# Performance work log

Hardware: AMD Instinct MI355X
Metric: run time of the kernel (lower is better)

Reference implementation:

```python
import jax, jax.numpy as jnp
import numpy as np

B, T, H, A = 64, 512, 1024, 300


def setup_inputs() -> dict:
    key = jax.random.key(0)
    ks = jax.random.split(key, 12)
    s = 0.02  # weight init scale
    return {
        "hidden": jax.random.normal(ks[0], (B, T, H), jnp.float32),
        "aspect": jax.random.normal(ks[1], (B, 1, A), jnp.float32),
        # torch Linear stores weight as [out_features, in_features]
        "W_h": jax.random.normal(ks[2], (H, H), jnp.float32) * s,
        "b_h": jax.random.normal(ks[3], (H,), jnp.float32) * s,
        "W_v": jax.random.normal(ks[4], (A, A), jnp.float32) * s,
        "b_v": jax.random.normal(ks[5], (A,), jnp.float32) * s,
        "w_w": jax.random.normal(ks[6], (1, H + A), jnp.float32) * s,
        "w_b": jax.random.normal(ks[7], (1,), jnp.float32) * s,
        "W_p": jax.random.normal(ks[8], (H, H), jnp.float32) * s,
        "b_p": jax.random.normal(ks[9], (H,), jnp.float32) * s,
        "W_x": jax.random.normal(ks[10], (H, H), jnp.float32) * s,
        "b_x": jax.random.normal(ks[11], (H,), jnp.float32) * s,
    }


def reference(hidden, aspect, W_h, b_h, W_v, b_v, w_w, w_b, W_p, b_p, W_x, b_x):
    # transformed aspect: [B, 1, A], repeated along seq dim -> [B, T, A]
    tv = aspect @ W_v.T + b_v
    rep_v = jnp.broadcast_to(tv, (hidden.shape[0], hidden.shape[1], tv.shape[-1]))
    # M = tanh(concat(W_h(hidden), repeated_v)) : [B, T, H+A]
    M = jnp.tanh(jnp.concatenate([hidden @ W_h.T + b_h, rep_v], axis=-1))
    # additive attention scores -> softmax over T
    scores = jnp.einsum("bts,os->bto", M, w_w)[..., 0] + w_b[0]  # [B, T]
    alpha = jax.nn.softmax(scores, axis=-1)
    # weighted sum r = alpha^T @ hidden : [B, 1, H]
    r = jnp.einsum("bt,bth->bh", alpha, hidden)[:, None, :]
    # NOTE: faithful to original torch broadcasting quirk:
    # [B,1,H] + [B,H] broadcasts to [B,B,H]
    output = jnp.tanh((r @ W_p.T + b_p) + (hidden[:, -1, :] @ W_x.T + b_x))
    return output
```

## Files before the change

### kernel.cpp

```cpp
#include <hip/hip_runtime.h>
#include <hip/hip_bf16.h>
#include <stdint.h>

#define B_DIM 64
#define T_DIM 512
#define H_DIM 1024
#define K_DIM 1024
#define M_DIM (B_DIM * T_DIM)

typedef __bf16 bf16x8 __attribute__((ext_vector_type(8)));
typedef float f32x4 __attribute__((ext_vector_type(4)));

__device__ __forceinline__ float tanh_fast(float x) {
  float e = __expf(2.0f * x);
  return 1.0f - 2.0f / (e + 1.0f);
}

__device__ __forceinline__ float bf2f(unsigned short u) {
  return __uint_as_float(((unsigned int)u) << 16);
}

__device__ __forceinline__ void async_cp16(const void* gp, void* lp) {
  __builtin_amdgcn_global_load_lds(
      reinterpret_cast<const __attribute__((address_space(1))) uint32_t*>(
          reinterpret_cast<uintptr_t>(gp)),
      reinterpret_cast<__attribute__((address_space(3))) uint32_t*>(
          reinterpret_cast<uintptr_t>(lp)),
      16, 0, 0);
}

__global__ void prep_kernel(const float* __restrict__ hidden, __bf16* __restrict__ hidBf,
                            const float* __restrict__ Wh, __bf16* __restrict__ whBf,
                            float* __restrict__ scores) {
  const int bid = blockIdx.x, tid = threadIdx.x;
  if (bid < 32768) {
    int i = bid * 256 + tid;
    float4 v = reinterpret_cast<const float4*>(hidden)[i];
    union { __bf16 b[4]; uint2 u; } o;
    o.b[0] = (__bf16)v.x; o.b[1] = (__bf16)v.y; o.b[2] = (__bf16)v.z; o.b[3] = (__bf16)v.w;
    reinterpret_cast<uint2*>(hidBf)[i] = o.u;
  } else if (bid < 33792) {
    int i = (bid - 32768) * 256 + tid;
    float4 v = reinterpret_cast<const float4*>(Wh)[i];
    union { __bf16 b[4]; uint2 u; } o;
    o.b[0] = (__bf16)v.x; o.b[1] = (__bf16)v.y; o.b[2] = (__bf16)v.z; o.b[3] = (__bf16)v.w;
    reinterpret_cast<uint2*>(whBf)[i] = o.u;
  } else {
    int i = (bid - 33792) * 256 + tid;
    reinterpret_cast<float4*>(scores)[i] = make_float4(0.f, 0.f, 0.f, 0.f);
  }
}

#define GM_BK 64
__global__ __launch_bounds__(256, 2) void gemm_scores_kernel(
    const __bf16* __restrict__ A, const __bf16* __restrict__ Bm,
    const float* __restrict__ bh, const float* __restrict__ ww,
    float* __restrict__ scores) {
  __shared__ __attribute__((aligned(16))) __bf16 lA[256 * GM_BK];
  __shared__ __attribute__((aligned(16))) __bf16 lB[128 * GM_BK];

  const int tid = threadIdx.x;
  const int bid = blockIdx.x;
  const int m0 = (bid & 127) * 256;
  const int n0 = (bid >> 7) * 128;

  const int wv = tid >> 6;
  const int lane = tid & 63;
  const int wm = wv & 1, wn = wv >> 1;
  const int r16 = lane & 15, quad = lane >> 4;

  f32x4 acc[8][4] = {};

  const __bf16* gA[8]; __bf16* lAd[8];
#pragma unroll
  for (int j = 0; j < 8; ++j) {
    int c = j * 256 + tid;
    int row = c >> 3;
    int p = c & 7;
    int kc = p ^ ((row >> 1) & 7);
    gA[j] = A + (size_t)(m0 + row) * K_DIM + kc * 8;
    lAd[j] = &lA[c * 8];
  }
  const __bf16* gB[4]; __bf16* lBd[4];
#pragma unroll
  for (int j = 0; j < 4; ++j) {
    int c = j * 256 + tid;
    int row = c >> 3;
    int p = c & 7;
    int kc = p ^ ((row >> 1) & 7);
    gB[j] = Bm + (size_t)(n0 + row) * K_DIM + kc * 8;
    lBd[j] = &lB[c * 8];
  }

  const int sw = r16 >> 1;
  const __bf16* pa[2]; const __bf16* pb[2];
#pragma unroll
  for (int kk = 0; kk < 2; ++kk) {
    pa[kk] = &lA[(wm * 128 + r16) * GM_BK + ((kk * 4 + quad) ^ sw) * 8];
    pb[kk] = &lB[(wn * 64 + r16) * GM_BK + ((kk * 4 + quad) ^ sw) * 8];
  }

#pragma unroll
  for (int k0 = 0; k0 < K_DIM; k0 += GM_BK) {
#pragma unroll
    for (int j = 0; j < 8; ++j) async_cp16(gA[j] + k0, lAd[j]);
#pragma unroll
    for (int j = 0; j < 4; ++j) async_cp16(gB[j] + k0, lBd[j]);
    __syncthreads();
#pragma unroll
    for (int kk = 0; kk < 2; ++kk) {
      bf16x8 bfr[4];
#pragma unroll
      for (int ni = 0; ni < 4; ++ni)
        bfr[ni] = *reinterpret_cast<const bf16x8*>(pb[kk] + ni * 16 * GM_BK);
      bf16x8 af[8];
#pragma unroll
      for (int mi = 0; mi < 8; ++mi)
        af[mi] = *reinterpret_cast<const bf16x8*>(pa[kk] + mi * 16 * GM_BK);
#pragma unroll
      for (int mi = 0; mi < 8; ++mi)
#pragma unroll
        for (int ni = 0; ni < 4; ++ni)
          acc[mi][ni] = __builtin_amdgcn_mfma_f32_16x16x32_bf16(af[mi], bfr[ni], acc[mi][ni], 0, 0, 0);
    }
    __syncthreads();
  }

  float bhv[4], wwv[4];
#pragma unroll
  for (int ni = 0; ni < 4; ++ni) {
    int n = n0 + wn * 64 + ni * 16 + r16;
    bhv[ni] = bh[n];
    wwv[ni] = ww[n];
  }
#pragma unroll
  for (int mi = 0; mi < 8; ++mi) {
#pragma unroll
    for (int rg = 0; rg < 4; ++rg) {
      float s = 0.f;
#pragma unroll
      for (int ni = 0; ni < 4; ++ni)
        s += tanh_fast(acc[mi][ni][rg] + bhv[ni]) * wwv[ni];
      s += __shfl_xor(s, 1, 16);
      s += __shfl_xor(s, 2, 16);
      s += __shfl_xor(s, 4, 16);
      s += __shfl_xor(s, 8, 16);
      if (r16 == 0) {
        int m = m0 + wm * 128 + mi * 16 + quad * 4 + rg;
        atomicAdd(&scores[m], s);
      }
    }
  }
}

__global__ void wsum_kernel(const float* __restrict__ scores,
                            const __bf16* __restrict__ hiddenBf,
                            float* __restrict__ r8) {
  __shared__ float al[64];
  __shared__ float red[8];
  const int bid = blockIdx.x, tid = threadIdx.x;
  const int b = bid >> 3, tc = bid & 7;
  const int wv = tid >> 6, lane = tid & 63;
  float v0 = scores[b * T_DIM + tid];
  float v1 = scores[b * T_DIM + 256 + tid];
  float mx = fmaxf(v0, v1);
#pragma unroll
  for (int off = 1; off < 64; off <<= 1) mx = fmaxf(mx, __shfl_xor(mx, off, 64));
  if (lane == 0) red[wv] = mx;
  __syncthreads();
  mx = fmaxf(fmaxf(red[0], red[1]), fmaxf(red[2], red[3]));
  float e0 = __expf(v0 - mx), e1 = __expf(v1 - mx);
  float s = e0 + e1;
#pragma unroll
  for (int off = 1; off < 64; off <<= 1) s += __shfl_xor(s, off, 64);
  if (lane == 0) red[4 + wv] = s;
  __syncthreads();
  float inv = 1.0f / (red[4] + red[5] + red[6] + red[7]);
  if (tid < 64) al[tid] = __expf(scores[b * T_DIM + tc * 64 + tid] - mx) * inv;
  __syncthreads();
  const __bf16* hp = hiddenBf + (size_t)b * T_DIM * H_DIM + (size_t)tc * 64 * H_DIM + tid * 4;
  float4 acc = make_float4(0.f, 0.f, 0.f, 0.f);
#pragma unroll 8
  for (int t = 0; t < 64; ++t) {
    float a = al[t];
    ushort4 u = *reinterpret_cast<const ushort4*>(hp + (size_t)t * H_DIM);
    acc.x += a * bf2f(u.x);
    acc.y += a * bf2f(u.y);
    acc.z += a * bf2f(u.z);
    acc.w += a * bf2f(u.w);
  }
  *reinterpret_cast<float4*>(r8 + (size_t)(b * 8 + tc) * H_DIM + tid * 4) = acc;
}

#define IG 4
__global__ void rowvec2_kernel(const float* __restrict__ r8,
                               const float* __restrict__ hidden,
                               const float* __restrict__ W_p, const float* __restrict__ b_p,
                               const float* __restrict__ W_x, const float* __restrict__ b_x,
                               float* __restrict__ rp, float* __restrict__ xq) {
  __shared__ __attribute__((aligned(16))) float sv[IG][H_DIM];
  const int h0 = blockIdx.x * 64;
  const int i0 = blockIdx.y * IG;
  const int which = blockIdx.z;
  const int tid = threadIdx.x;
  const float* W = which ? W_x : W_p;
  const float* bias = which ? b_x : b_p;
  float* dst = which ? xq : rp;
  if (which == 0) {
#pragma unroll
    for (int ii = 0; ii < IG; ++ii) {
      const float* src = r8 + (size_t)(i0 + ii) * 8 * H_DIM + tid * 4;
      float4 a = *reinterpret_cast<const float4*>(src);
#pragma unroll
      for (int tc = 1; tc < 8; ++tc) {
        float4 v = *reinterpret_cast<const float4*>(src + (size_t)tc * H_DIM);
        a.x += v.x; a.y += v.y; a.z += v.z; a.w += v.w;
      }
      *reinterpret_cast<float4*>(&sv[ii][tid * 4]) = a;
    }
  } else {
#pragma unroll
    for (int ii = 0; ii < IG; ++ii) {
      const float* src = hidden + (size_t)(i0 + ii) * T_DIM * H_DIM +
                         (size_t)(T_DIM - 1) * H_DIM + tid * 4;
      *reinterpret_cast<float4*>(&sv[ii][tid * 4]) = *reinterpret_cast<const float4*>(src);
    }
  }
  __syncthreads();
  const int hl = tid >> 2;
  const int kq = tid & 3;
  const float* wr = W + (size_t)(h0 + hl) * H_DIM + kq * 4;
  float acc[IG] = {};
#pragma unroll 8
  for (int j = 0; j < 64; ++j) {
    float4 w4 = *reinterpret_cast<const float4*>(wr + j * 16);
#pragma unroll
    for (int ii = 0; ii < IG; ++ii) {
      float4 s4 = *reinterpret_cast<const float4*>(&sv[ii][kq * 4 + j * 16]);
      acc[ii] += w4.x * s4.x + w4.y * s4.y + w4.z * s4.z + w4.w * s4.w;
    }
  }
#pragma unroll
  for (int ii = 0; ii < IG; ++ii) {
    acc[ii] += __shfl_xor(acc[ii], 1, 4);
    acc[ii] += __shfl_xor(acc[ii], 2, 4);
  }
  if (kq == 0) {
    float bb = bias[h0 + hl];
#pragma unroll
    for (int ii = 0; ii < IG; ++ii)
      dst[(size_t)(i0 + ii) * H_DIM + h0 + hl] = acc[ii] + bb;
  }
}

__global__ void final_kernel(const float* __restrict__ rp, const float* __restrict__ xq,
                             float* __restrict__ out) {
  int idx = blockIdx.x * 256 + threadIdx.x;
  int e = idx * 4;
  int i = e >> 16;
  int j = (e >> 10) & 63;
  int h = e & 1023;
  float4 a = *reinterpret_cast<const float4*>(&rp[i * H_DIM + h]);
  float4 b = *reinterpret_cast<const float4*>(&xq[j * H_DIM + h]);
  float4 o;
  o.x = tanh_fast(a.x + b.x);
  o.y = tanh_fast(a.y + b.y);
  o.z = tanh_fast(a.z + b.z);
  o.w = tanh_fast(a.w + b.w);
  *reinterpret_cast<float4*>(&out[e]) = o;
}

extern "C" void kernel_launch(void* const* d_in, const int* in_sizes, int n_in,
                              void* d_out, int out_size, void* d_ws, size_t ws_size,
                              hipStream_t stream) {
  const float* hidden = (const float*)d_in[0];
  const float* W_h = (const float*)d_in[2];
  const float* b_h = (const float*)d_in[3];
  const float* w_w = (const float*)d_in[6];
  const float* W_p = (const float*)d_in[8];
  const float* b_p = (const float*)d_in[9];
  const float* W_x = (const float*)d_in[10];
  const float* b_x = (const float*)d_in[11];
  float* out = (float*)d_out;

  char* ws = (char*)d_ws;
  __bf16* hidBf = (__bf16*)ws;
  __bf16* whBf = (__bf16*)(ws + 67108864);
  float* r8 = (float*)(ws + 67108864);
  float* scores = (float*)(ws + 69206016);
  float* rpB = (float*)(ws + 69337088);
  float* xqB = (float*)(ws + 69599232);

  prep_kernel<<<33824, 256, 0, stream>>>(hidden, hidBf, W_h, whBf, scores);

  gemm_scores_kernel<<<1024, 256, 0, stream>>>(hidBf, whBf, b_h, w_w, scores);

  wsum_kernel<<<512, 256, 0, stream>>>(scores, hidBf, r8);

  rowvec2_kernel<<<dim3(H_DIM / 64, B_DIM / IG, 2), 256, 0, stream>>>(
      r8, hidden, W_p, b_p, W_x, b_x, rpB, xqB);

  final_kernel<<<(B_DIM * B_DIM * H_DIM / 4) / 256, 256, 0, stream>>>(rpB, xqB, out);
}
```

Before: 344.3 us.

## Fuse all stages into one persistent kernel with grid-wide barriers

Replaces the five separate launches (convert, GEMM+scores, softmax-weighted sum, row-vector GEMVs, final tanh) with a single persistent kernel of 512 blocks. The stages are separated by atomic-counter grid barriers, and shared memory is reused through a union. Each block now loops over two GEMM tiles and over grid-strided chunks for the elementwise phases. The aim is to remove kernel launch gaps and tail effects between stages. In exchange it relies on all blocks being co-resident, adds a memset launch for the counters, and the barrier spin has a timeout that could silently break ordering.

```diff
diff --git a/kernel.cpp b/kernel.cpp
--- a/kernel.cpp
+++ b/kernel.cpp
@@ -7,6 +7,10 @@
 #define H_DIM 1024
 #define K_DIM 1024
 #define M_DIM (B_DIM * T_DIM)
+#define GM_BK 64
+#define IG 4
+#define NBLK 512
+#define NTHR (NBLK * 256)
 
 typedef __bf16 bf16x8 __attribute__((ext_vector_type(8)));
 typedef float f32x4 __attribute__((ext_vector_type(4)));
@@ -29,245 +33,277 @@
       16, 0, 0);
 }
 
-__global__ void prep_kernel(const float* __restrict__ hidden, __bf16* __restrict__ hidBf,
-                            const float* __restrict__ Wh, __bf16* __restrict__ whBf,
-                            float* __restrict__ scores) {
-  const int bid = blockIdx.x, tid = threadIdx.x;
-  if (bid < 32768) {
-    int i = bid * 256 + tid;
-    float4 v = reinterpret_cast<const float4*>(hidden)[i];
-    union { __bf16 b[4]; uint2 u; } o;
-    o.b[0] = (__bf16)v.x; o.b[1] = (__bf16)v.y; o.b[2] = (__bf16)v.z; o.b[3] = (__bf16)v.w;
-    reinterpret_cast<uint2*>(hidBf)[i] = o.u;
-  } else if (bid < 33792) {
-    int i = (bid - 32768) * 256 + tid;
-    float4 v = reinterpret_cast<const float4*>(Wh)[i];
-    union { __bf16 b[4]; uint2 u; } o;
-    o.b[0] = (__bf16)v.x; o.b[1] = (__bf16)v.y; o.b[2] = (__bf16)v.z; o.b[3] = (__bf16)v.w;
-    reinterpret_cast<uint2*>(whBf)[i] = o.u;
-  } else {
-    int i = (bid - 33792) * 256 + tid;
-    reinterpret_cast<float4*>(scores)[i] = make_float4(0.f, 0.f, 0.f, 0.f);
-  }
-}
-
-#define GM_BK 64
-__global__ __launch_bounds__(256, 2) void gemm_scores_kernel(
-    const __bf16* __restrict__ A, const __bf16* __restrict__ Bm,
-    const float* __restrict__ bh, const float* __restrict__ ww,
-    float* __restrict__ scores) {
-  __shared__ __attribute__((aligned(16))) __bf16 lA[256 * GM_BK];
-  __shared__ __attribute__((aligned(16))) __bf16 lB[128 * GM_BK];
-
+__device__ __forceinline__ void cvt4(const float4& v, uint2* dst) {
+  union { __bf16 b[4]; uint2 u; } o;
+  o.b[0] = (__bf16)v.x; o.b[1] = (__bf16)v.y; o.b[2] = (__bf16)v.z; o.b[3] = (__bf16)v.w;
+  *dst = o.u;
+}
+
+__device__ __forceinline__ void grid_barrier(unsigned* cnt, int k) {
+  __syncthreads();
+  if (threadIdx.x == 0) {
+    __threadfence();
+    __hip_atomic_fetch_add(&cnt[k], 1u, __ATOMIC_RELEASE, __HIP_MEMORY_SCOPE_AGENT);
+    unsigned spins = 0;
+    while (__hip_atomic_load(&cnt[k], __ATOMIC_ACQUIRE, __HIP_MEMORY_SCOPE_AGENT) <
+           (unsigned)NBLK) {
+      __builtin_amdgcn_s_sleep(8);
+      if (++spins > (1u << 20)) break;
+    }
+    __threadfence();
+  }
+  __syncthreads();
+}
+
+union SharedU {
+  struct { __bf16 lA[256 * GM_BK]; __bf16 lB[128 * GM_BK]; } g;
+  struct { float al[64]; float red[8]; } w;
+  float sv[IG][H_DIM];
+};
+
+__global__ __launch_bounds__(256, 2) void mega_kernel(
+    const float* __restrict__ hidden, __bf16* __restrict__ hidBf,
+    const float* __restrict__ W_h, __bf16* __restrict__ whBf,
+    float* __restrict__ scores, const float* __restrict__ b_h,
+    const float* __restrict__ w_w, float* __restrict__ r8,
+    const float* __restrict__ W_p, const float* __restrict__ b_p,
+    const float* __restrict__ W_x, const float* __restrict__ b_x,
+    float* __restrict__ rp, float* __restrict__ xq, float* __restrict__ out,
+    unsigned* __restrict__ barcnt) {
+  __shared__ __attribute__((aligned(16))) SharedU sh;
   const int tid = threadIdx.x;
   const int bid = blockIdx.x;
-  const int m0 = (bid & 127) * 256;
-  const int n0 = (bid >> 7) * 128;
-
-  const int wv = tid >> 6;
-  const int lane = tid & 63;
-  const int wm = wv & 1, wn = wv >> 1;
-  const int r16 = lane & 15, quad = lane >> 4;
-
-  f32x4 acc[8][4] = {};
-
-  const __bf16* gA[8]; __bf16* lAd[8];
-#pragma unroll
-  for (int j = 0; j < 8; ++j) {
-    int c = j * 256 + tid;
-    int row = c >> 3;
-    int p = c & 7;
-    int kc = p ^ ((row >> 1) & 7);
-    gA[j] = A + (size_t)(m0 + row) * K_DIM + kc * 8;
-    lAd[j] = &lA[c * 8];
-  }
-  const __bf16* gB[4]; __bf16* lBd[4];
-#pragma unroll
-  for (int j = 0; j < 4; ++j) {
-    int c = j * 256 + tid;
-    int row = c >> 3;
-    int p = c & 7;
-    int kc = p ^ ((row >> 1) & 7);
-    gB[j] = Bm + (size_t)(n0 + row) * K_DIM + kc * 8;
-    lBd[j] = &lB[c * 8];
-  }
-
-  const int sw = r16 >> 1;
-  const __bf16* pa[2]; const __bf16* pb[2];
-#pragma unroll
-  for (int kk = 0; kk < 2; ++kk) {
-    pa[kk] = &lA[(wm * 128 + r16) * GM_BK + ((kk * 4 + quad) ^ sw) * 8];
-    pb[kk] = &lB[(wn * 64 + r16) * GM_BK + ((kk * 4 + quad) ^ sw) * 8];
-  }
-
-#pragma unroll
-  for (int k0 = 0; k0 < K_DIM; k0 += GM_BK) {
-#pragma unroll
-    for (int j = 0; j < 8; ++j) async_cp16(gA[j] + k0, lAd[j]);
-#pragma unroll
-    for (int j = 0; j < 4; ++j) async_cp16(gB[j] + k0, lBd[j]);
+  const int gt = bid * 256 + tid;
+
+  {
+    const float4* hs = reinterpret_cast<const float4*>(hidden);
+    uint2* hd = reinterpret_cast<uint2*>(hidBf);
+#pragma unroll 4
+    for (int it = 0; it < 64; ++it) {
+      int i = it * NTHR + gt;
+      float4 v = hs[i];
+      cvt4(v, &hd[i]);
+    }
+    const float4* wsrc = reinterpret_cast<const float4*>(W_h);
+    uint2* wd = reinterpret_cast<uint2*>(whBf);
+#pragma unroll
+    for (int it = 0; it < 2; ++it) {
+      int i = it * NTHR + gt;
+      float4 v = wsrc[i];
+      cvt4(v, &wd[i]);
+    }
+    if (gt < 8192) reinterpret_cast<float4*>(scores)[gt] = make_float4(0.f, 0.f, 0.f, 0.f);
+  }
+  grid_barrier(barcnt, 0);
+
+  {
+    const int wv = tid >> 6;
+    const int lane = tid & 63;
+    const int wm = wv & 1, wn = wv >> 1;
+    const int r16 = lane & 15, quad = lane >> 4;
+    const int sw = r16 >> 1;
+
+    __bf16* lAd[8]; int rowA[8], kcA[8];
+#pragma unroll
+    for (int j = 0; j < 8; ++j) {
+      int c = j * 256 + tid;
+      rowA[j] = c >> 3;
+      kcA[j] = (c & 7) ^ ((rowA[j] >> 1) & 7);
+      lAd[j] = &sh.g.lA[c * 8];
+    }
+    __bf16* lBd[4]; int rowB[4], kcB[4];
+#pragma unroll
+    for (int j = 0; j < 4; ++j) {
+      int c = j * 256 + tid;
+      rowB[j] = c >> 3;
+      kcB[j] = (c & 7) ^ ((rowB[j] >> 1) & 7);
+      lBd[j] = &sh.g.lB[c * 8];
+    }
+    const __bf16* pa[2]; const __bf16* pb[2];
+#pragma unroll
+    for (int kk = 0; kk < 2; ++kk) {
+      pa[kk] = &sh.g.lA[(wm * 128 + r16) * GM_BK + ((kk * 4 + quad) ^ sw) * 8];
+      pb[kk] = &sh.g.lB[(wn * 64 + r16) * GM_BK + ((kk * 4 + quad) ^ sw) * 8];
+    }
+
+#pragma unroll 1
+    for (int tpass = 0; tpass < 2; ++tpass) {
+      const int tt = bid + tpass * NBLK;
+      const int m0 = (tt & 127) * 256;
+      const int n0 = (tt >> 7) * 128;
+
+      const __bf16* gA[8];
+#pragma unroll
+      for (int j = 0; j < 8; ++j) gA[j] = hidBf + (size_t)(m0 + rowA[j]) * K_DIM + kcA[j] * 8;
+      const __bf16* gB[4];
+#pragma unroll
+      for (int j = 0; j < 4; ++j) gB[j] = whBf + (size_t)(n0 + rowB[j]) * K_DIM + kcB[j] * 8;
+
+      f32x4 acc[8][4] = {};
+
+#pragma unroll
+      for (int k0 = 0; k0 < K_DIM; k0 += GM_BK) {
+#pragma unroll
+        for (int j = 0; j < 8; ++j) async_cp16(gA[j] + k0, lAd[j]);
+#pragma unroll
+        for (int j = 0; j < 4; ++j) async_cp16(gB[j] + k0, lBd[j]);
+        __syncthreads();
+#pragma unroll
+        for (int kk = 0; kk < 2; ++kk) {
+          bf16x8 bfr[4];
+#pragma unroll
+          for (int ni = 0; ni < 4; ++ni)
+            bfr[ni] = *reinterpret_cast<const bf16x8*>(pb[kk] + ni * 16 * GM_BK);
+          bf16x8 af[8];
+#pragma unroll
+          for (int mi = 0; mi < 8; ++mi)
+            af[mi] = *reinterpret_cast<const bf16x8*>(pa[kk] + mi * 16 * GM_BK);
+#pragma unroll
+          for (int mi = 0; mi < 8; ++mi)
+#pragma unroll
+            for (int ni = 0; ni < 4; ++ni)
+              acc[mi][ni] = __builtin_amdgcn_mfma_f32_16x16x32_bf16(af[mi], bfr[ni], acc[mi][ni], 0, 0, 0);
+        }
+        __syncthreads();
+      }
+
+      float bhv[4], wwv[4];
+#pragma unroll
+      for (int ni = 0; ni < 4; ++ni) {
+        int n = n0 + wn * 64 + ni * 16 + r16;
+        bhv[ni] = b_h[n];
+        wwv[ni] = w_w[n];
+      }
+#pragma unroll
+      for (int mi = 0; mi < 8; ++mi) {
+#pragma unroll
+        for (int rg = 0; rg < 4; ++rg) {
+          float s = 0.f;
+#pragma unroll
+          for (int ni = 0; ni < 4; ++ni)
+            s += tanh_fast(acc[mi][ni][rg] + bhv[ni]) * wwv[ni];
+          s += __shfl_xor(s, 1, 16);
+          s += __shfl_xor(s, 2, 16);
+          s += __shfl_xor(s, 4, 16);
+          s += __shfl_xor(s, 8, 16);
+          if (r16 == 0) {
+            int m = m0 + wm * 128 + mi * 16 + quad * 4 + rg;
+            atomicAdd(&scores[m], s);
+          }
+        }
+      }
+    }
+  }
+  grid_barrier(barcnt, 1);
+
+  {
+    const int b = bid >> 3, tc = bid & 7;
+    const int wv = tid >> 6, lane = tid & 63;
+    float v0 = scores[b * T_DIM + tid];
+    float v1 = scores[b * T_DIM + 256 + tid];
+    float mx = fmaxf(v0, v1);
+#pragma unroll
+    for (int off = 1; off < 64; off <<= 1) mx = fmaxf(mx, __shfl_xor(mx, off, 64));
+    if (lane == 0) sh.w.red[wv] = mx;
     __syncthreads();
-#pragma unroll
-    for (int kk = 0; kk < 2; ++kk) {
-      bf16x8 bfr[4];
-#pragma unroll
-      for (int ni = 0; ni < 4; ++ni)
-        bfr[ni] = *reinterpret_cast<const bf16x8*>(pb[kk] + ni * 16 * GM_BK);
-      bf16x8 af[8];
-#pragma unroll
-      for (int mi = 0; mi < 8; ++mi)
-        af[mi] = *reinterpret_cast<const bf16x8*>(pa[kk] + mi * 16 * GM_BK);
-#pragma unroll
-      for (int mi = 0; mi < 8; ++mi)
-#pragma unroll
-        for (int ni = 0; ni < 4; ++ni)
-          acc[mi][ni] = __builtin_amdgcn_mfma_f32_16x16x32_bf16(af[mi], bfr[ni], acc[mi][ni], 0, 0, 0);
-    }
+    mx = fmaxf(fmaxf(sh.w.red[0], sh.w.red[1]), fmaxf(sh.w.red[2], sh.w.red[3]));
+    float e0 = __expf(v0 - mx), e1 = __expf(v1 - mx);
+    float s = e0 + e1;
+#pragma unroll
+    for (int off = 1; off < 64; off <<= 1) s += __shfl_xor(s, off, 64);
+    if (lane == 0) sh.w.red[4 + wv] = s;
     __syncthreads();
-  }
-
-  float bhv[4], wwv[4];
-#pragma unroll
-  for (int ni = 0; ni < 4; ++ni) {
-    int n = n0 + wn * 64 + ni * 16 + r16;
-    bhv[ni] = bh[n];
-    wwv[ni] = ww[n];
-  }
-#pragma unroll
-  for (int mi = 0; mi < 8; ++mi) {
-#pragma unroll
-    for (int rg = 0; rg < 4; ++rg) {
-      float s = 0.f;
-#pragma unroll
-      for (int ni = 0; ni < 4; ++ni)
-        s += tanh_fast(acc[mi][ni][rg] + bhv[ni]) * wwv[ni];
-      s += __shfl_xor(s, 1, 16);
-      s += __shfl_xor(s, 2, 16);
-      s += __shfl_xor(s, 4, 16);
-      s += __shfl_xor(s, 8, 16);
-      if (r16 == 0) {
-        int m = m0 + wm * 128 + mi * 16 + quad * 4 + rg;
-        atomicAdd(&scores[m], s);
-      }
-    }
-  }
-}
-
-__global__ void wsum_kernel(const float* __restrict__ scores,
-                            const __bf16* __restrict__ hiddenBf,
-                            float* __restrict__ r8) {
-  __shared__ float al[64];
-  __shared__ float red[8];
-  const int bid = blockIdx.x, tid = threadIdx.x;
-  const int b = bid >> 3, tc = bid & 7;
-  const int wv = tid >> 6, lane = tid & 63;
-  float v0 = scores[b * T_DIM + tid];
-  float v1 = scores[b * T_DIM + 256 + tid];
-  float mx = fmaxf(v0, v1);
-#pragma unroll
-  for (int off = 1; off < 64; off <<= 1) mx = fmaxf(mx, __shfl_xor(mx, off, 64));
-  if (lane == 0) red[wv] = mx;
-  __syncthreads();
-  mx = fmaxf(fmaxf(red[0], red[1]), fmaxf(red[2], red[3]));
-  float e0 = __expf(v0 - mx), e1 = __expf(v1 - mx);
-  float s = e0 + e1;
-#pragma unroll
-  for (int off = 1; off < 64; off <<= 1) s += __shfl_xor(s, off, 64);
-  if (lane == 0) red[4 + wv] = s;
-  __syncthreads();
-  float inv = 1.0f / (red[4] + red[5] + red[6] + red[7]);
-  if (tid < 64) al[tid] = __expf(scores[b * T_DIM + tc * 64 + tid] - mx) * inv;
-  __syncthreads();
-  const __bf16* hp = hiddenBf + (size_t)b * T_DIM * H_DIM + (size_t)tc * 64 * H_DIM + tid * 4;
-  float4 acc = make_float4(0.f, 0.f, 0.f, 0.f);
+    float inv = 1.0f / (sh.w.red[4] + sh.w.red[5] + sh.w.red[6] + sh.w.red[7]);
+    if (tid < 64) sh.w.al[tid] = __expf(scores[b * T_DIM + tc * 64 + tid] - mx) * inv;
+    __syncthreads();
+    const __bf16* hp = hidBf + (size_t)b * T_DIM * H_DIM + (size_t)tc * 64 * H_DIM + tid * 4;
+    float4 acc = make_float4(0.f, 0.f, 0.f, 0.f);
 #pragma unroll 8
-  for (int t = 0; t < 64; ++t) {
-    float a = al[t];
-    ushort4 u = *reinterpret_cast<const ushort4*>(hp + (size_t)t * H_DIM);
-    acc.x += a * bf2f(u.x);
-    acc.y += a * bf2f(u.y);
-    acc.z += a * bf2f(u.z);
-    acc.w += a * bf2f(u.w);
-  }
-  *reinterpret_cast<float4*>(r8 + (size_t)(b * 8 + tc) * H_DIM + tid * 4) = acc;
-}
-
-#define IG 4
-__global__ void rowvec2_kernel(const float* __restrict__ r8,
-                               const float* __restrict__ hidden,
-                               const float* __restrict__ W_p, const float* __restrict__ b_p,
-                               const float* __restrict__ W_x, const float* __restrict__ b_x,
-                               float* __restrict__ rp, float* __restrict__ xq) {
-  __shared__ __attribute__((aligned(16))) float sv[IG][H_DIM];
-  const int h0 = blockIdx.x * 64;
-  const int i0 = blockIdx.y * IG;
-  const int which = blockIdx.z;
-  const int tid = threadIdx.x;
-  const float* W = which ? W_x : W_p;
-  const float* bias = which ? b_x : b_p;
-  float* dst = which ? xq : rp;
-  if (which == 0) {
+    for (int t = 0; t < 64; ++t) {
+      float a = sh.w.al[t];
+      ushort4 u = *reinterpret_cast<const ushort4*>(hp + (size_t)t * H_DIM);
+      acc.x += a * bf2f(u.x);
+      acc.y += a * bf2f(u.y);
+      acc.z += a * bf2f(u.z);
+      acc.w += a * bf2f(u.w);
+    }
+    *reinterpret_cast<float4*>(r8 + (size_t)(b * 8 + tc) * H_DIM + tid * 4) = acc;
+  }
+  grid_barrier(barcnt, 2);
+
+  {
+    const int h0 = (bid & 15) * 64;
+    const int i0 = ((bid >> 4) & 15) * IG;
+    const int which = bid >> 8;
+    const float* W = which ? W_x : W_p;
+    const float* bias = which ? b_x : b_p;
+    float* dst = which ? xq : rp;
+    if (which == 0) {
+#pragma unroll
+      for (int ii = 0; ii < IG; ++ii) {
+        const float* src = r8 + (size_t)(i0 + ii) * 8 * H_DIM + tid * 4;
+        float4 a = *reinterpret_cast<const float4*>(src);
+#pragma unroll
+        for (int tc = 1; tc < 8; ++tc) {
+          float4 v = *reinterpret_cast<const float4*>(src + (size_t)tc * H_DIM);
+          a.x += v.x; a.y += v.y; a.z += v.z; a.w += v.w;
+        }
+        *reinterpret_cast<float4*>(&sh.sv[ii][tid * 4]) = a;
+      }
+    } else {
+#pragma unroll
+      for (int ii = 0; ii < IG; ++ii) {
+        const float* src = hidden + (size_t)(i0 + ii) * T_DIM * H_DIM +
+                           (size_t)(T_DIM - 1) * H_DIM + tid * 4;
+        *reinterpret_cast<float4*>(&sh.sv[ii][tid * 4]) = *reinterpret_cast<const float4*>(src);
+      }
+    }
+    __syncthreads();
+    const int hl = tid >> 2;
+    const int kq = tid & 3;
+    const float* wr = W + (size_t)(h0 + hl) * H_DIM + kq * 4;
+    float acc[IG] = {};
+#pragma unroll 8
+    for (int j = 0; j < 64; ++j) {
+      float4 w4 = *reinterpret_cast<const float4*>(wr + j * 16);
+#pragma unroll
+      for (int ii = 0; ii < IG; ++ii) {
+        float4 s4 = *reinterpret_cast<const float4*>(&sh.sv[ii][kq * 4 + j * 16]);
+        acc[ii] += w4.x * s4.x + w4.y * s4.y + w4.z * s4.z + w4.w * s4.w;
+      }
+    }
 #pragma unroll
     for (int ii = 0; ii < IG; ++ii) {
-      const float* src = r8 + (size_t)(i0 + ii) * 8 * H_DIM + tid * 4;
-      float4 a = *reinterpret_cast<const float4*>(src);
-#pragma unroll
-      for (int tc = 1; tc < 8; ++tc) {
-        float4 v = *reinterpret_cast<const float4*>(src + (size_t)tc * H_DIM);
-        a.x += v.x; a.y += v.y; a.z += v.z; a.w += v.w;
-      }
-      *reinterpret_cast<float4*>(&sv[ii][tid * 4]) = a;
-    }
-  } else {
-#pragma unroll
-    for (int ii = 0; ii < IG; ++ii) {
-      const float* src = hidden + (size_t)(i0 + ii) * T_DIM * H_DIM +
-                         (size_t)(T_DIM - 1) * H_DIM + tid * 4;
-      *reinterpret_cast<float4*>(&sv[ii][tid * 4]) = *reinterpret_cast<const float4*>(src);
-    }
-  }
-  __syncthreads();
-  const int hl = tid >> 2;
-  const int kq = tid & 3;
-  const float* wr = W + (size_t)(h0 + hl) * H_DIM + kq * 4;
-  float acc[IG] = {};
-#pragma unroll 8
-  for (int j = 0; j < 64; ++j) {
-    float4 w4 = *reinterpret_cast<const float4*>(wr + j * 16);
-#pragma unroll
-    for (int ii = 0; ii < IG; ++ii) {
-      float4 s4 = *reinterpret_cast<const float4*>(&sv[ii][kq * 4 + j * 16]);
-      acc[ii] += w4.x * s4.x + w4.y * s4.y + w4.z * s4.z + w4.w * s4.w;
-    }
-  }
-#pragma unroll
-  for (int ii = 0; ii < IG; ++ii) {
-    acc[ii] += __shfl_xor(acc[ii], 1, 4);
-    acc[ii] += __shfl_xor(acc[ii], 2, 4);
-  }
-  if (kq == 0) {
-    float bb = bias[h0 + hl];
-#pragma unroll
-    for (int ii = 0; ii < IG; ++ii)
-      dst[(size_t)(i0 + ii) * H_DIM + h0 + hl] = acc[ii] + bb;
-  }
-}
-
-__global__ void final_kernel(const float* __restrict__ rp, const float* __restrict__ xq,
-                             float* __restrict__ out) {
-  int idx = blockIdx.x * 256 + threadIdx.x;
-  int e = idx * 4;
-  int i = e >> 16;
-  int j = (e >> 10) & 63;
-  int h = e & 1023;
-  float4 a = *reinterpret_cast<const float4*>(&rp[i * H_DIM + h]);
-  float4 b = *reinterpret_cast<const float4*>(&xq[j * H_DIM + h]);
-  float4 o;
-  o.x = tanh_fast(a.x + b.x);
-  o.y = tanh_fast(a.y + b.y);
-  o.z = tanh_fast(a.z + b.z);
-  o.w = tanh_fast(a.w + b.w);
-  *reinterpret_cast<float4*>(&out[e]) = o;
+      acc[ii] += __shfl_xor(acc[ii], 1, 4);
+      acc[ii] += __shfl_xor(acc[ii], 2, 4);
+    }
+    if (kq == 0) {
+      float bb = bias[h0 + hl];
+#pragma unroll
+      for (int ii = 0; ii < IG; ++ii)
+        dst[(size_t)(i0 + ii) * H_DIM + h0 + hl] = acc[ii] + bb;
+    }
+  }
+  grid_barrier(barcnt, 3);
+
+  {
+#pragma unroll
+    for (int it = 0; it < 8; ++it) {
+      int idx = it * NTHR + gt;
+      int e = idx * 4;
+      int i = e >> 16;
+      int j = (e >> 10) & 63;
+      int h = e & 1023;
+      float4 a = *reinterpret_cast<const float4*>(&rp[i * H_DIM + h]);
+      float4 b = *reinterpret_cast<const float4*>(&xq[j * H_DIM + h]);
+      float4 o;
+      o.x = tanh_fast(a.x + b.x);
+      o.y = tanh_fast(a.y + b.y);
+      o.z = tanh_fast(a.z + b.z);
+      o.w = tanh_fast(a.w + b.w);
+      *reinterpret_cast<float4*>(&out[e]) = o;
+    }
+  }
 }
 
 extern "C" void kernel_launch(void* const* d_in, const int* in_sizes, int n_in,
@@ -290,15 +326,11 @@
   float* scores = (float*)(ws + 69206016);
   float* rpB = (float*)(ws + 69337088);
   float* xqB = (float*)(ws + 69599232);
-
-  prep_kernel<<<33824, 256, 0, stream>>>(hidden, hidBf, W_h, whBf, scores);
-
-  gemm_scores_kernel<<<1024, 256, 0, stream>>>(hidBf, whBf, b_h, w_w, scores);
-
-  wsum_kernel<<<512, 256, 0, stream>>>(scores, hidBf, r8);
-
-  rowvec2_kernel<<<dim3(H_DIM / 64, B_DIM / IG, 2), 256, 0, stream>>>(
-      r8, hidden, W_p, b_p, W_x, b_x, rpB, xqB);
-
-  final_kernel<<<(B_DIM * B_DIM * H_DIM / 4) / 256, 256, 0, stream>>>(rpB, xqB, out);
-}
+  unsigned* barcnt = (unsigned*)(ws + 69861376);
+
+  hipMemsetAsync(barcnt, 0, 64, stream);
+
+  mega_kernel<<<NBLK, 256, 0, stream>>>(hidden, hidBf, W_h, whBf, scores, b_h,
+                                        w_w, r8, W_p, b_p, W_x, b_x, rpB, xqB,
+                                        out, barcnt);
+}
```

New measurement: 1.034 ms. 200% more time.
